# Kernel tuning notes

Measured on AMD Instinct MI355X. Metric: run time of the kernel, lower is better.

## Reference

```python
import jax, jax.numpy as jnp
import numpy as np

N = 8192
IN_DIM, HID_DIM, OUT_DIM = 32, 64, 16


def setup_inputs() -> dict:
    key = jax.random.key(0)
    k1, k2, k3, k4, k5, k6, k7 = jax.random.split(key, 7)
    s1 = 1.0 / np.sqrt(IN_DIM)
    s2 = 1.0 / np.sqrt(HID_DIM)
    return {
        "adj1": jax.random.normal(k1, (N, N), jnp.float32),
        "adj2": jax.random.normal(k2, (N, N), jnp.float32),
        "features": jax.random.normal(k3, (N, IN_DIM), jnp.float32),
        # gc1 linear (shared across both aggregation branches)
        "W1": jax.random.uniform(k4, (IN_DIM, HID_DIM), jnp.float32, -s1, s1),
        "b1": jax.random.uniform(k5, (HID_DIM,), jnp.float32, -s1, s1),
        # gc2 linear
        "W2": jax.random.uniform(k6, (HID_DIM, OUT_DIM), jnp.float32, -s2, s2),
        "b2": jax.random.uniform(k7, (OUT_DIM,), jnp.float32, -s2, s2),
    }


def _gc_layer(adj1, adj2, x, W, b):
    # branch 1: aggregate -> shared linear -> relu
    o1 = jax.nn.relu(jnp.matmul(adj1, x) @ W + b)
    # branch 2: same linear weights
    o2 = jax.nn.relu(jnp.matmul(adj2, x) @ W + b)
    return o1 + o2


def reference(adj1, adj2, features, W1, b1, W2, b2):
    h1 = _gc_layer(adj1, adj2, features, W1, b1)  # [N, HID_DIM]
    h2 = _gc_layer(adj1, adj2, h1, W2, b2)        # [N, OUT_DIM]
    return h2
```

## Files before the change

kernel.cpp:

```cpp
#include <hip/hip_runtime.h>
#include <stdint.h>

#define NN 8192
#define IN_DIM 32
#define HID_DIM 64
#define OUT_DIM 16

typedef __attribute__((ext_vector_type(8))) short short8;
typedef __attribute__((ext_vector_type(4))) float f32x4;

__device__ __forceinline__ short f2bf_bits(float x){
  uint32_t u = __builtin_bit_cast(uint32_t, x);
  u += 0x7FFFu + ((u >> 16) & 1u);
  return (short)(u >> 16);
}

__device__ __forceinline__ short8 cvt8(f32x4 lo, f32x4 hi){
  short8 r;
  r[0]=f2bf_bits(lo[0]); r[1]=f2bf_bits(lo[1]); r[2]=f2bf_bits(lo[2]); r[3]=f2bf_bits(lo[3]);
  r[4]=f2bf_bits(hi[0]); r[5]=f2bf_bits(hi[1]); r[6]=f2bf_bits(hi[2]); r[7]=f2bf_bits(hi[3]);
  return r;
}

__global__ __launch_bounds__(256) void k_g(const float* __restrict__ X, const float* __restrict__ W1,
                                           short* __restrict__ Gt){
  const int b    = blockIdx.x;
  const int rb   = (b & 127) * 64;
  const int cg   = b >> 7;
  const int lane = threadIdx.x & 63;
  const int c    = cg * 4 + (threadIdx.x >> 6);
  const int r    = rb + lane;
  const float* xr = X + (size_t)r * IN_DIM;
  float acc = 0.f;
  #pragma unroll
  for (int k = 0; k < IN_DIM; ++k)
    acc += xr[k] * W1[(size_t)k * HID_DIM + c];
  Gt[(size_t)c * NN + r] = f2bf_bits(acc);
}

template<int REV>
__global__ __launch_bounds__(256) void mm_db(const float* __restrict__ adj1, const float* __restrict__ adj2,
                                             const short* __restrict__ Bt,
                                             float* __restrict__ P1, float* __restrict__ P2, int klen){
  __shared__ __align__(16) float sA[2][2][64 * 64];
  const int tid  = threadIdx.x;
  const int lane = tid & 63;
  const int wave = tid >> 6;
  const int bm   = REV ? ((int)gridDim.x - 1 - (int)blockIdx.x) : (int)blockIdx.x;
  const int ks   = REV ? ((int)gridDim.y - 1 - (int)blockIdx.y) : (int)blockIdx.y;
  const int k0   = ks * klen;
  const int ngrp = klen >> 6;

  const int srow = tid >> 4;
  const int sg   = (tid & 15) ^ (srow & 7);
  const size_t growb = (size_t)(bm * 64) * NN;

  const int rl = wave * 16 + (lane & 15);
  const int sw = lane & 7;
  const int qh = lane >> 4;

  f32x4 acc1[4] = {{0,0,0,0},{0,0,0,0},{0,0,0,0},{0,0,0,0}};
  f32x4 acc2[4] = {{0,0,0,0},{0,0,0,0},{0,0,0,0},{0,0,0,0}};

  auto stage = [&](int t){
    const int g     = REV ? (ngrp - 1 - t) : t;
    const int buf   = t & 1;
    const size_t colb = (size_t)(k0 + g * 64) + (size_t)sg * 4;
    #pragma unroll
    for (int p = 0; p < 4; ++p){
      const float* s1 = adj1 + growb + (size_t)(p * 16 + srow) * NN + colb;
      const float* s2 = adj2 + growb + (size_t)(p * 16 + srow) * NN + colb;
      __builtin_amdgcn_global_load_lds(
          (const __attribute__((address_space(1))) void*)s1,
          (__attribute__((address_space(3))) void*)&sA[buf][0][p * 1024 + tid * 4], 16, 0, 0);
      __builtin_amdgcn_global_load_lds(
          (const __attribute__((address_space(1))) void*)s2,
          (__attribute__((address_space(3))) void*)&sA[buf][1][p * 1024 + tid * 4], 16, 0, 0);
    }
  };

  stage(0);
  __syncthreads();

  #pragma unroll 1
  for (int gi = 0; gi < ngrp; ++gi){
    if (gi + 1 < ngrp) stage(gi + 1);

    const int g     = REV ? (ngrp - 1 - gi) : gi;
    const int buf   = gi & 1;
    const int kbase = k0 + g * 64;
    #pragma unroll
    for (int j = 0; j < 2; ++j){
      const int gr0 = j * 8 + qh * 2;
      const int o0  = rl * 64 + ((gr0     ^ sw) << 2);
      const int o1  = rl * 64 + (((gr0+1) ^ sw) << 2);
      f32x4 lo1 = *(const f32x4*)&sA[buf][0][o0];
      f32x4 hi1 = *(const f32x4*)&sA[buf][0][o1];
      f32x4 lo2 = *(const f32x4*)&sA[buf][1][o0];
      f32x4 hi2 = *(const f32x4*)&sA[buf][1][o1];
      short8 b[4];
      const size_t bk = (size_t)kbase + j * 32 + qh * 8;
      #pragma unroll
      for (int f = 0; f < 4; ++f)
        b[f] = *(const short8*)(Bt + (size_t)(f * 16 + (lane & 15)) * NN + bk);
      short8 fa1 = cvt8(lo1, hi1);
      short8 fa2 = cvt8(lo2, hi2);
      #pragma unroll
      for (int f = 0; f < 4; ++f){
        acc1[f] = __builtin_amdgcn_mfma_f32_16x16x32_bf16(fa1, b[f], acc1[f], 0, 0, 0);
        acc2[f] = __builtin_amdgcn_mfma_f32_16x16x32_bf16(fa2, b[f], acc2[f], 0, 0, 0);
      }
    }
    __syncthreads();
  }

  const int orow = bm * 64 + wave * 16 + qh * 4;
  const int col  = lane & 15;
  float* p1 = P1 + ((size_t)ks * NN + orow) * HID_DIM + col;
  float* p2 = P2 + ((size_t)ks * NN + orow) * HID_DIM + col;
  #pragma unroll
  for (int r = 0; r < 4; ++r){
    #pragma unroll
    for (int f = 0; f < 4; ++f){
      p1[(size_t)r * HID_DIM + f * 16] = acc1[f][r];
      p2[(size_t)r * HID_DIM + f * 16] = acc2[f][r];
    }
  }
}

__global__ __launch_bounds__(256) void l1_combine(const float* __restrict__ Y1p, const float* __restrict__ Y2p,
                                                  const float* __restrict__ b1,
                                                  short* __restrict__ H1t, int S){
  __shared__ float sH[64][65];
  const int tid = threadIdx.x, lane = tid & 63, wave = tid >> 6;
  const int rb = blockIdx.x * 64;
  const float bc = b1[lane];
  #pragma unroll 4
  for (int rq = 0; rq < 16; ++rq){
    const int r = rq * 4 + wave;
    const int row = rb + r;
    float s1 = 0.f, s2 = 0.f;
    for (int sp = 0; sp < S; ++sp){
      s1 += Y1p[((size_t)sp * NN + row) * HID_DIM + lane];
      s2 += Y2p[((size_t)sp * NN + row) * HID_DIM + lane];
    }
    sH[r][lane] = fmaxf(s1 + bc, 0.f) + fmaxf(s2 + bc, 0.f);
  }
  __syncthreads();
  #pragma unroll 4
  for (int i = 0; i < 16; ++i){
    const int c = wave * 16 + i;
    H1t[(size_t)c * NN + rb + lane] = f2bf_bits(sH[lane][c]);
  }
}

__global__ __launch_bounds__(256) void l2_combine(const float* __restrict__ Z1p, const float* __restrict__ Z2p,
                                                  const float* __restrict__ W2, const float* __restrict__ b2,
                                                  float* __restrict__ out, int S){
  __shared__ float sW[HID_DIM * OUT_DIM];
  __shared__ float sb[OUT_DIM];
  __shared__ float sz[4][2][HID_DIM];
  const int tid = threadIdx.x;
  for (int i = tid; i < HID_DIM * OUT_DIM; i += 256) sW[i] = W2[i];
  if (tid < OUT_DIM) sb[tid] = b2[tid];
  const int sub = tid >> 6, t = tid & 63;
  const int row = blockIdx.x * 4 + sub;
  float s1 = 0.f, s2 = 0.f;
  for (int sp = 0; sp < S; ++sp){
    s1 += Z1p[((size_t)sp * NN + row) * HID_DIM + t];
    s2 += Z2p[((size_t)sp * NN + row) * HID_DIM + t];
  }
  sz[sub][0][t] = s1;
  sz[sub][1][t] = s2;
  __syncthreads();
  if (t < OUT_DIM){
    float a = sb[t], b = sb[t];
    #pragma unroll
    for (int k = 0; k < HID_DIM; ++k){
      a += sz[sub][0][k] * sW[k * OUT_DIM + t];
      b += sz[sub][1][k] * sW[k * OUT_DIM + t];
    }
    out[(size_t)row * OUT_DIM + t] = fmaxf(a, 0.f) + fmaxf(b, 0.f);
  }
}

extern "C" void kernel_launch(void* const* d_in, const int* in_sizes, int n_in,
                              void* d_out, int out_size, void* d_ws, size_t ws_size,
                              hipStream_t stream){
  const float* adj1 = (const float*)d_in[0];
  const float* adj2 = (const float*)d_in[1];
  const float* X    = (const float*)d_in[2];
  const float* W1   = (const float*)d_in[3];
  const float* b1   = (const float*)d_in[4];
  const float* W2   = (const float*)d_in[5];
  const float* b2   = (const float*)d_in[6];
  float* out = (float*)d_out;

  char* ws = (char*)d_ws;
  short* Gt  = (short*)ws;
  short* H1t = (short*)(ws + (size_t)1024 * 1024);
  const size_t off = (size_t)2 * 1024 * 1024;

  int S = 4;
  while (S > 1 && off + (size_t)S * 4 * 1024 * 1024 > ws_size) S >>= 1;
  float* P1 = (float*)(ws + off);
  float* P2 = P1 + (size_t)S * NN * HID_DIM;
  const int klen = NN / S;

  k_g        <<<dim3(2048),       dim3(256), 0, stream>>>(X, W1, Gt);
  mm_db<0>   <<<dim3(NN / 64, S), dim3(256), 0, stream>>>(adj1, adj2, Gt, P1, P2, klen);
  l1_combine <<<dim3(NN / 64),    dim3(256), 0, stream>>>(P1, P2, b1, H1t, S);
  mm_db<1>   <<<dim3(NN / 64, S), dim3(256), 0, stream>>>(adj1, adj2, H1t, P1, P2, klen);
  l2_combine <<<dim3(NN / 4),     dim3(256), 0, stream>>>(P1, P2, W2, b2, out, S);
}
```

Baseline: 260.8 us.

## Split adjacency matmul by matrix and stage wider 256-column row tiles

```diff
diff --git a/kernel.cpp b/kernel.cpp
--- a/kernel.cpp
+++ b/kernel.cpp
@@ -39,92 +39,82 @@
 }
 
 template<int REV>
-__global__ __launch_bounds__(256) void mm_db(const float* __restrict__ adj1, const float* __restrict__ adj2,
-                                             const short* __restrict__ Bt,
-                                             float* __restrict__ P1, float* __restrict__ P2, int klen){
-  __shared__ __align__(16) float sA[2][2][64 * 64];
+__global__ __launch_bounds__(256) void mm_row(const float* __restrict__ adj1, const float* __restrict__ adj2,
+                                              const short* __restrict__ Bt,
+                                              float* __restrict__ P1, float* __restrict__ P2, int klen){
+  __shared__ __align__(16) float sA[2][64 * 256];
   const int tid  = threadIdx.x;
   const int lane = tid & 63;
   const int wave = tid >> 6;
   const int bm   = REV ? ((int)gridDim.x - 1 - (int)blockIdx.x) : (int)blockIdx.x;
   const int ks   = REV ? ((int)gridDim.y - 1 - (int)blockIdx.y) : (int)blockIdx.y;
+  const float* __restrict__ adj = blockIdx.z ? adj2 : adj1;
   const int k0   = ks * klen;
-  const int ngrp = klen >> 6;
-
-  const int srow = tid >> 4;
-  const int sg   = (tid & 15) ^ (srow & 7);
+  const int ngrp = klen >> 8;
+  const int skew = bm & (ngrp - 1);
   const size_t growb = (size_t)(bm * 64) * NN;
 
-  const int rl = wave * 16 + (lane & 15);
-  const int sw = lane & 7;
+  const int rl = lane & 15;
   const int qh = lane >> 4;
 
-  f32x4 acc1[4] = {{0,0,0,0},{0,0,0,0},{0,0,0,0},{0,0,0,0}};
-  f32x4 acc2[4] = {{0,0,0,0},{0,0,0,0},{0,0,0,0},{0,0,0,0}};
+  auto gat = [&](int t){
+    int s = REV ? (skew + ngrp - 1 - t) : (skew + t);
+    return s & (ngrp - 1);
+  };
 
   auto stage = [&](int t){
-    const int g     = REV ? (ngrp - 1 - t) : t;
-    const int buf   = t & 1;
-    const size_t colb = (size_t)(k0 + g * 64) + (size_t)sg * 4;
-    #pragma unroll
-    for (int p = 0; p < 4; ++p){
-      const float* s1 = adj1 + growb + (size_t)(p * 16 + srow) * NN + colb;
-      const float* s2 = adj2 + growb + (size_t)(p * 16 + srow) * NN + colb;
+    const int g   = gat(t);
+    const int buf = t & 1;
+    const size_t colb = (size_t)(k0 + g * 256);
+    #pragma unroll
+    for (int p = 0; p < 16; ++p){
+      const int row = p * 4 + wave;
+      const int key = row & 15;
+      const float* src = adj + growb + (size_t)row * NN + colb + ((lane ^ key) << 2);
       __builtin_amdgcn_global_load_lds(
-          (const __attribute__((address_space(1))) void*)s1,
-          (__attribute__((address_space(3))) void*)&sA[buf][0][p * 1024 + tid * 4], 16, 0, 0);
-      __builtin_amdgcn_global_load_lds(
-          (const __attribute__((address_space(1))) void*)s2,
-          (__attribute__((address_space(3))) void*)&sA[buf][1][p * 1024 + tid * 4], 16, 0, 0);
+          (const __attribute__((address_space(1))) void*)src,
+          (__attribute__((address_space(3))) void*)&sA[buf][row * 256 + lane * 4], 16, 0, 0);
     }
   };
+
+  f32x4 acc[4] = {{0,0,0,0},{0,0,0,0},{0,0,0,0},{0,0,0,0}};
 
   stage(0);
   __syncthreads();
 
   #pragma unroll 1
-  for (int gi = 0; gi < ngrp; ++gi){
-    if (gi + 1 < ngrp) stage(gi + 1);
-
-    const int g     = REV ? (ngrp - 1 - gi) : gi;
-    const int buf   = gi & 1;
-    const int kbase = k0 + g * 64;
-    #pragma unroll
-    for (int j = 0; j < 2; ++j){
-      const int gr0 = j * 8 + qh * 2;
-      const int o0  = rl * 64 + ((gr0     ^ sw) << 2);
-      const int o1  = rl * 64 + (((gr0+1) ^ sw) << 2);
-      f32x4 lo1 = *(const f32x4*)&sA[buf][0][o0];
-      f32x4 hi1 = *(const f32x4*)&sA[buf][0][o1];
-      f32x4 lo2 = *(const f32x4*)&sA[buf][1][o0];
-      f32x4 hi2 = *(const f32x4*)&sA[buf][1][o1];
+  for (int t = 0; t < ngrp; ++t){
+    if (t + 1 < ngrp) stage(t + 1);
+    const int g     = gat(t);
+    const int buf   = t & 1;
+    const int kbase = k0 + g * 256;
+    const int rbase = (wave * 16 + rl) * 256;
+    #pragma unroll
+    for (int j = 0; j < 8; ++j){
+      const int g0 = j * 8 + qh * 2;
+      f32x4 lo = *(const f32x4*)&sA[buf][rbase + (((g0    ) ^ rl) << 2)];
+      f32x4 hi = *(const f32x4*)&sA[buf][rbase + (((g0 + 1) ^ rl) << 2)];
       short8 b[4];
       const size_t bk = (size_t)kbase + j * 32 + qh * 8;
       #pragma unroll
       for (int f = 0; f < 4; ++f)
-        b[f] = *(const short8*)(Bt + (size_t)(f * 16 + (lane & 15)) * NN + bk);
-      short8 fa1 = cvt8(lo1, hi1);
-      short8 fa2 = cvt8(lo2, hi2);
+        b[f] = *(const short8*)(Bt + (size_t)(f * 16 + rl) * NN + bk);
+      short8 fa = cvt8(lo, hi);
       #pragma unroll
-      for (int f = 0; f < 4; ++f){
-        acc1[f] = __builtin_amdgcn_mfma_f32_16x16x32_bf16(fa1, b[f], acc1[f], 0, 0, 0);
-        acc2[f] = __builtin_amdgcn_mfma_f32_16x16x32_bf16(fa2, b[f], acc2[f], 0, 0, 0);
-      }
+      for (int f = 0; f < 4; ++f)
+        acc[f] = __builtin_amdgcn_mfma_f32_16x16x32_bf16(fa, b[f], acc[f], 0, 0, 0);
     }
     __syncthreads();
   }
 
   const int orow = bm * 64 + wave * 16 + qh * 4;
-  const int col  = lane & 15;
-  float* p1 = P1 + ((size_t)ks * NN + orow) * HID_DIM + col;
-  float* p2 = P2 + ((size_t)ks * NN + orow) * HID_DIM + col;
+  float* P = blockIdx.z ? P2 : P1;
+  float* p = P + ((size_t)ks * NN + orow) * HID_DIM + rl;
   #pragma unroll
   for (int r = 0; r < 4; ++r){
     #pragma unroll
-    for (int f = 0; f < 4; ++f){
-      p1[(size_t)r * HID_DIM + f * 16] = acc1[f][r];
-      p2[(size_t)r * HID_DIM + f * 16] = acc2[f][r];
-    }
+    for (int f = 0; f < 4; ++f)
+      p[(size_t)r * HID_DIM + f * 16] = acc[f][r];
   }
 }
 
@@ -207,9 +197,9 @@
   float* P2 = P1 + (size_t)S * NN * HID_DIM;
   const int klen = NN / S;
 
-  k_g        <<<dim3(2048),       dim3(256), 0, stream>>>(X, W1, Gt);
-  mm_db<0>   <<<dim3(NN / 64, S), dim3(256), 0, stream>>>(adj1, adj2, Gt, P1, P2, klen);
-  l1_combine <<<dim3(NN / 64),    dim3(256), 0, stream>>>(P1, P2, b1, H1t, S);
-  mm_db<1>   <<<dim3(NN / 64, S), dim3(256), 0, stream>>>(adj1, adj2, H1t, P1, P2, klen);
-  l2_combine <<<dim3(NN / 4),     dim3(256), 0, stream>>>(P1, P2, W2, b2, out, S);
-}
+  k_g        <<<dim3(2048),          dim3(256), 0, stream>>>(X, W1, Gt);
+  mm_row<0>  <<<dim3(NN / 64, S, 2), dim3(256), 0, stream>>>(adj1, adj2, Gt, P1, P2, klen);
+  l1_combine <<<dim3(NN / 64),       dim3(256), 0, stream>>>(P1, P2, b1, H1t, S);
+  mm_row<1>  <<<dim3(NN / 64, S, 2), dim3(256), 0, stream>>>(adj1, adj2, H1t, P1, P2, klen);
+  l2_combine <<<dim3(NN / 4),        dim3(256), 0, stream>>>(P1, P2, W2, b2, out, S);
+}
```

Measured after the change: 492.2 us. +88.7%, slower.
